# Kernel optimization log

Measured on AMD Instinct MI355X. Metric: run time of the kernel, lower is better.

Reference implementation:

```python
import jax, jax.numpy as jnp
import numpy as np

K, N = 4096, 4096
GROUP_SIZE = 64
N_GROUPS = N // GROUP_SIZE
B, S = 4, 2048
NBITS = 4


def setup_inputs() -> dict:
    key = jax.random.key(0)
    ks = jax.random.split(key, 7)
    x = jax.random.normal(ks[0], (B, S, N), dtype=jnp.float32)
    # per-group scales/zeros broadcast over the group_size axis
    scales = jax.random.uniform(ks[1], (K, N_GROUPS, 1), dtype=jnp.float32, minval=0.001, maxval=0.05)
    zeros = jax.random.uniform(ks[2], (K, N_GROUPS, 1), dtype=jnp.float32, minval=0.0, maxval=2.0 ** NBITS - 1)
    mu1 = jax.random.uniform(ks[3], (N,), dtype=jnp.float32, minval=0.5, maxval=1.5)
    mu2 = jax.random.uniform(ks[4], (K,), dtype=jnp.float32, minval=0.5, maxval=1.5)
    bias = jax.random.normal(ks[5], (K,), dtype=jnp.float32)
    W_q = jax.random.randint(ks[6], (K, N), 0, 2 ** NBITS, dtype=jnp.int32)
    return {"x": x, "scales": scales, "zeros": zeros, "mu1": mu1, "mu2": mu2, "bias": bias, "W_q": W_q}


def reference(x, scales, zeros, mu1, mu2, bias, W_q):
    # dequantize: per-group (Q - zero) * scale, then Sinkhorn rescale mu2 (rows) * mu1 (cols)
    k, n = W_q.shape
    n_groups = scales.shape[1]
    Qg = W_q.astype(jnp.float32).reshape(k, n_groups, -1)  # [K, G, gs]
    W_deq = ((Qg - zeros) * scales).reshape(k, n) * mu2[:, None] * mu1[None, :]
    W_deq = W_deq.astype(x.dtype)
    # nn.functional.linear: x @ W^T + b
    return jnp.einsum('bsn,kn->bsk', x, W_deq) + bias
```

## Files before the change

### kernel.cpp

```cpp
#include <hip/hip_runtime.h>
#include <hip/hip_bf16.h>
#include <stdint.h>
#include <type_traits>

typedef unsigned short u16;
typedef __bf16 bf16x8 __attribute__((ext_vector_type(8)));
typedef float f32x4 __attribute__((ext_vector_type(4)));

#define M_TOT 8192
#define N_TOT 4096
#define K_TOT 4096
#define BM 256
#define BN 256
#define BK 64
#define NT 64

#define HALF_EL 8192
#define B_OFF   16384
#define SLOT_EL 32768
#define SLOT_BYTES 65536

#define CVT_BLOCKS 16384
#define DEQ_BLOCKS 8192

template <int V> using ic = std::integral_constant<int, V>;
template <bool V> using bc = std::integral_constant<bool, V>;

__device__ __forceinline__ u16 f2bf(float f) {
    union { float f; uint32_t u; } v; v.f = f;
    uint32_t u = v.u;
    return (u16)((u + 0x7fffu + ((u >> 16) & 1u)) >> 16);
}

__global__ __launch_bounds__(256) void prep_kernel(const float* __restrict__ x,
                                                   u16* __restrict__ xb,
                                                   const int* __restrict__ wq,
                                                   const float* __restrict__ scales,
                                                   const float* __restrict__ zeros,
                                                   const float* __restrict__ mu1,
                                                   const float* __restrict__ mu2,
                                                   u16* __restrict__ wb) {
    const int b = blockIdx.x;
    if (b < CVT_BLOCKS) {
        const int i = b * 256 + threadIdx.x;
        const float4* p = (const float4*)x + (size_t)i * 2;
        float4 v0 = p[0], v1 = p[1];
        uint4 o;
        o.x = (uint32_t)f2bf(v0.x) | ((uint32_t)f2bf(v0.y) << 16);
        o.y = (uint32_t)f2bf(v0.z) | ((uint32_t)f2bf(v0.w) << 16);
        o.z = (uint32_t)f2bf(v1.x) | ((uint32_t)f2bf(v1.y) << 16);
        o.w = (uint32_t)f2bf(v1.z) | ((uint32_t)f2bf(v1.w) << 16);
        *((uint4*)(xb + (size_t)i * 8)) = o;
    } else {
        const int i = (b - CVT_BLOCKS) * 256 + threadIdx.x;
        const int k  = i >> 9;
        const int n0 = (i & 511) << 3;
        const int g  = n0 >> 6;
        const float z  = zeros[k * 64 + g];
        const float sm = scales[k * 64 + g] * mu2[k];
        const int4* qp = (const int4*)(wq + (size_t)k * N_TOT + n0);
        int4 q0 = qp[0], q1 = qp[1];
        const float4* mp = (const float4*)(mu1 + n0);
        float4 u0 = mp[0], u1 = mp[1];
        uint4 o;
        o.x = (uint32_t)f2bf(((float)q0.x - z) * sm * u0.x) |
              ((uint32_t)f2bf(((float)q0.y - z) * sm * u0.y) << 16);
        o.y = (uint32_t)f2bf(((float)q0.z - z) * sm * u0.z) |
              ((uint32_t)f2bf(((float)q0.w - z) * sm * u0.w) << 16);
        o.z = (uint32_t)f2bf(((float)q1.x - z) * sm * u1.x) |
              ((uint32_t)f2bf(((float)q1.y - z) * sm * u1.y) << 16);
        o.w = (uint32_t)f2bf(((float)q1.z - z) * sm * u1.z) |
              ((uint32_t)f2bf(((float)q1.w - z) * sm * u1.w) << 16);
        *((uint4*)(wb + (size_t)k * N_TOT + n0)) = o;
    }
}

__global__ __launch_bounds__(512, 2) void gemm_kernel(const u16* __restrict__ Xb,
                                                      const u16* __restrict__ Wb,
                                                      const float* __restrict__ bias,
                                                      float* __restrict__ out) {
    __shared__ __align__(16) u16 lds[2 * SLOT_EL];

    const int bid = blockIdx.x;
    const int cpx = gridDim.x >> 3;
    const int swz = (bid & 7) * cpx + (bid >> 3);
    const int bm = swz >> 4;
    const int bn = swz & 15;

    const int tid  = threadIdx.x;
    const int w    = tid >> 6;
    const int lane = tid & 63;
    const int wm = w >> 2, wn = w & 3;

    const int scol = (((lane & 7) ^ (lane >> 3)) << 3);
    const u16* aT = Xb + (size_t)(bm * BM + w * 16 + (lane >> 3)) * N_TOT + scol;
    const u16* bT = Wb + (size_t)(bn * BN + w * 16 + (lane >> 3)) * N_TOT + scol;

    u16* const sdA = &lds[w * 1024];
    u16* const sdB = &lds[B_OFF + w * 1024];

    auto gload = [](const u16* s, u16* d) {
        __builtin_amdgcn_global_load_lds(
            (const __attribute__((address_space(1))) uint32_t*)s,
            (__attribute__((address_space(3))) uint32_t*)d, 16, 0, 0);
    };
    auto stA = [&](auto SlC, auto Hc, auto Dc) {
        const u16* s = aT + (size_t)(Hc.value * 128) * N_TOT + Dc.value;
        u16* d = sdA + SlC.value * SLOT_EL + Hc.value * HALF_EL;
        gload(s, d); gload(s + (size_t)8 * N_TOT, d + 512);
    };
    auto stB = [&](auto SlC, auto Hc, auto Dc) {
        const u16* s = bT + (size_t)(Hc.value * 128) * N_TOT + Dc.value;
        u16* d = sdB + SlC.value * SLOT_EL + Hc.value * HALF_EL;
        gload(s, d); gload(s + (size_t)8 * N_TOT, d + 512);
    };

    const int cc0 = (((lane >> 4) << 3)) ^ ((lane & 7) << 3);
    const int rA  = ((wm << 4) + (lane & 15)) << 6;
    const int rB  = ((wn << 4) + (lane & 15)) << 6;
    int oAa = (rA + cc0) * 2;
    int oAb = (rA + (cc0 ^ 32)) * 2;
    int oBa = (B_OFF + rB + cc0) * 2;
    int oBb = (B_OFF + rB + (cc0 ^ 32)) * 2;
    const char* const ldsc = (const char*)lds;

    f32x4 acc[2][2][4][2] = {};
    bf16x8 afLo[4][2], afHi[4][2];
    bf16x8 bf0[2][2], bf1[2][2];

    auto rd_afLo_next = [&]() {
        const int xa = oAa ^ SLOT_BYTES, xb2 = oAb ^ SLOT_BYTES;
        #pragma unroll
        for (int j = 0; j < 4; ++j) {
            afLo[j][0] = *(const bf16x8*)(ldsc + xa + j * 4096);
            afLo[j][1] = *(const bf16x8*)(ldsc + xb2 + j * 4096);
        }
    };
    auto rd_bf0_next = [&]() {
        const int xa = oBa ^ SLOT_BYTES, xb2 = oBb ^ SLOT_BYTES;
        #pragma unroll
        for (int j2 = 0; j2 < 2; ++j2) {
            bf0[j2][0] = *(const bf16x8*)(ldsc + xa + j2 * 8192);
            bf0[j2][1] = *(const bf16x8*)(ldsc + xb2 + j2 * 8192);
        }
    };
    auto rd_afHi_cur = [&]() {
        #pragma unroll
        for (int j = 0; j < 4; ++j) {
            afHi[j][0] = *(const bf16x8*)(ldsc + oAa + 16384 + j * 4096);
            afHi[j][1] = *(const bf16x8*)(ldsc + oAb + 16384 + j * 4096);
        }
    };
    auto rd_bf1_cur = [&]() {
        #pragma unroll
        for (int j2 = 0; j2 < 2; ++j2) {
            bf1[j2][0] = *(const bf16x8*)(ldsc + oBa + 16384 + j2 * 8192);
            bf1[j2][1] = *(const bf16x8*)(ldsc + oBb + 16384 + j2 * 8192);
        }
    };

    #define MFMA_CLUSTER(A, B, MH, NH)                                          \
        __builtin_amdgcn_s_setprio(1);                                          \
        _Pragma("unroll")                                                       \
        for (int ks = 0; ks < 2; ++ks)                                          \
            _Pragma("unroll")                                                   \
            for (int j = 0; j < 4; ++j)                                         \
                _Pragma("unroll")                                               \
                for (int j2 = 0; j2 < 2; ++j2)                                  \
                    acc[MH][NH][j][j2] = __builtin_amdgcn_mfma_f32_16x16x32_bf16(\
                        A[j][ks], B[j2][ks], acc[MH][NH][j][j2], 0, 0, 0);      \
        __builtin_amdgcn_s_setprio(0);

    auto ktile = [&](auto SlC, auto St0, auto St2, auto RdN,
                     auto V1c, auto V3c, auto D0, auto D1) {
        constexpr int SL = SlC.value;
        rd_bf1_cur();
        if constexpr (St0.value) { stA(ic<SL ^ 1>{}, ic<1>{}, D0);
                                   stB(ic<SL ^ 1>{}, ic<1>{}, D0); }
        MFMA_CLUSTER(afLo, bf0, 0, 0)
        rd_afHi_cur();
        MFMA_CLUSTER(afLo, bf1, 0, 1)
        if constexpr (V1c.value == 4) asm volatile("s_waitcnt vmcnt(4)" ::: "memory");
        else if constexpr (V1c.value == 0) asm volatile("s_waitcnt vmcnt(0)" ::: "memory");
        __builtin_amdgcn_s_barrier();
        __builtin_amdgcn_sched_barrier(0);
        if constexpr (RdN.value) rd_afLo_next();
        if constexpr (St2.value) { stA(SlC, ic<0>{}, D1);
                                   stB(SlC, ic<0>{}, D1); }
        MFMA_CLUSTER(afHi, bf1, 1, 1)
        MFMA_CLUSTER(afHi, bf0, 1, 0)
        if constexpr (RdN.value) rd_bf0_next();
        if constexpr (V3c.value == 4) asm volatile("s_waitcnt vmcnt(4)" ::: "memory");
        else if constexpr (V3c.value == 0) asm volatile("s_waitcnt vmcnt(0)" ::: "memory");
        __builtin_amdgcn_s_barrier();
        __builtin_amdgcn_sched_barrier(0);
        oAa ^= SLOT_BYTES; oAb ^= SLOT_BYTES; oBa ^= SLOT_BYTES; oBb ^= SLOT_BYTES;
    };

    stA(ic<0>{}, ic<0>{}, ic<0>{});  stB(ic<0>{}, ic<0>{}, ic<0>{});
    stA(ic<0>{}, ic<1>{}, ic<0>{});  stB(ic<0>{}, ic<1>{}, ic<0>{});
    stA(ic<1>{}, ic<0>{}, ic<BK>{}); stB(ic<1>{}, ic<0>{}, ic<BK>{});
    asm volatile("s_waitcnt vmcnt(4)" ::: "memory");
    __builtin_amdgcn_s_barrier();
    __builtin_amdgcn_sched_barrier(0);
    {
        #pragma unroll
        for (int j = 0; j < 4; ++j) {
            afLo[j][0] = *(const bf16x8*)(ldsc + oAa + j * 4096);
            afLo[j][1] = *(const bf16x8*)(ldsc + oAb + j * 4096);
        }
        #pragma unroll
        for (int j2 = 0; j2 < 2; ++j2) {
            bf0[j2][0] = *(const bf16x8*)(ldsc + oBa + j2 * 8192);
            bf0[j2][1] = *(const bf16x8*)(ldsc + oBb + j2 * 8192);
        }
    }

    for (int it = 0; it < 31; ++it) {
        ktile(ic<0>{}, bc<true>{}, bc<true>{}, bc<true>{},
              ic<4>{}, ic<4>{}, ic<BK>{}, ic<2 * BK>{});
        ktile(ic<1>{}, bc<true>{}, bc<true>{}, bc<true>{},
              ic<4>{}, ic<4>{}, ic<2 * BK>{}, ic<3 * BK>{});
        aT += 2 * BK;
        bT += 2 * BK;
    }
    ktile(ic<0>{}, bc<true>{}, bc<false>{}, bc<true>{},
          ic<4>{}, ic<0>{}, ic<BK>{}, ic<0>{});
    ktile(ic<1>{}, bc<false>{}, bc<false>{}, bc<false>{},
          ic<-1>{}, ic<-1>{}, ic<0>{}, ic<0>{});

    #undef MFMA_CLUSTER

    #pragma unroll
    for (int mh_ = 0; mh_ < 2; ++mh_)
        #pragma unroll
        for (int j = 0; j < 4; ++j)
            #pragma unroll
            for (int rr = 0; rr < 4; ++rr) {
                const int row = bm * BM + mh_ * 128 + j * 32 + wm * 16 + ((lane >> 4) << 2) + rr;
                float* orow = out + (size_t)row * K_TOT;
                #pragma unroll
                for (int nh_ = 0; nh_ < 2; ++nh_)
                    #pragma unroll
                    for (int j2 = 0; j2 < 2; ++j2) {
                        const int col = bn * BN + nh_ * 128 + j2 * 64 + wn * 16 + (lane & 15);
                        orow[col] = acc[mh_][nh_][j][j2][rr] + bias[col];
                    }
            }
}

extern "C" void kernel_launch(void* const* d_in, const int* in_sizes, int n_in,
                              void* d_out, int out_size, void* d_ws, size_t ws_size,
                              hipStream_t stream) {
    const float* x      = (const float*)d_in[0];
    const float* scales = (const float*)d_in[1];
    const float* zeros  = (const float*)d_in[2];
    const float* mu1    = (const float*)d_in[3];
    const float* mu2    = (const float*)d_in[4];
    const float* bias   = (const float*)d_in[5];
    const int*   wq     = (const int*)d_in[6];
    float* out = (float*)d_out;

    u16* xb = (u16*)d_ws;
    u16* wb = (u16*)d_ws + (size_t)M_TOT * N_TOT;

    prep_kernel<<<CVT_BLOCKS + DEQ_BLOCKS, 256, 0, stream>>>(
        x, xb, wq, scales, zeros, mu1, mu2, wb);
    gemm_kernel<<<(M_TOT / BM) * (K_TOT / BN), 512, 0, stream>>>(xb, wb, bias, out);
}
```

Measured before the change: 264.9 us.

## Load weight operand directly from global into registers, stage only activations in LDS

The W tile is no longer staged through shared memory. Each wave now reads its B fragments straight from global memory into registers, one k-tile ahead, while only the X tile stays double-buffered in LDS. This halves LDS use and removes the B shared-memory writes, reads and the explicit vmcnt waits. In exchange, B loads are duplicated across waves that share columns, their latency is exposed to the compiler's own wait insertion, and the async A loads lose their explicit wait-count control.

```diff
diff --git a/kernel.cpp b/kernel.cpp
--- a/kernel.cpp
+++ b/kernel.cpp
@@ -16,9 +16,8 @@
 #define NT 64
 
 #define HALF_EL 8192
-#define B_OFF   16384
-#define SLOT_EL 32768
-#define SLOT_BYTES 65536
+#define ASLOT_EL 16384
+#define ASLOT_BYTES 32768
 
 #define CVT_BLOCKS 16384
 #define DEQ_BLOCKS 8192
@@ -79,7 +78,7 @@
                                                       const u16* __restrict__ Wb,
                                                       const float* __restrict__ bias,
                                                       float* __restrict__ out) {
-    __shared__ __align__(16) u16 lds[2 * SLOT_EL];
+    __shared__ __align__(16) u16 lds[2 * ASLOT_EL];
 
     const int bid = blockIdx.x;
     const int cpx = gridDim.x >> 3;
@@ -94,10 +93,8 @@
 
     const int scol = (((lane & 7) ^ (lane >> 3)) << 3);
     const u16* aT = Xb + (size_t)(bm * BM + w * 16 + (lane >> 3)) * N_TOT + scol;
-    const u16* bT = Wb + (size_t)(bn * BN + w * 16 + (lane >> 3)) * N_TOT + scol;
 
     u16* const sdA = &lds[w * 1024];
-    u16* const sdB = &lds[B_OFF + w * 1024];
 
     auto gload = [](const u16* s, u16* d) {
         __builtin_amdgcn_global_load_lds(
@@ -106,44 +103,34 @@
     };
     auto stA = [&](auto SlC, auto Hc, auto Dc) {
         const u16* s = aT + (size_t)(Hc.value * 128) * N_TOT + Dc.value;
-        u16* d = sdA + SlC.value * SLOT_EL + Hc.value * HALF_EL;
-        gload(s, d); gload(s + (size_t)8 * N_TOT, d + 512);
-    };
-    auto stB = [&](auto SlC, auto Hc, auto Dc) {
-        const u16* s = bT + (size_t)(Hc.value * 128) * N_TOT + Dc.value;
-        u16* d = sdB + SlC.value * SLOT_EL + Hc.value * HALF_EL;
+        u16* d = sdA + SlC.value * ASLOT_EL + Hc.value * HALF_EL;
         gload(s, d); gload(s + (size_t)8 * N_TOT, d + 512);
     };
 
     const int cc0 = (((lane >> 4) << 3)) ^ ((lane & 7) << 3);
     const int rA  = ((wm << 4) + (lane & 15)) << 6;
-    const int rB  = ((wn << 4) + (lane & 15)) << 6;
     int oAa = (rA + cc0) * 2;
     int oAb = (rA + (cc0 ^ 32)) * 2;
-    int oBa = (B_OFF + rB + cc0) * 2;
-    int oBb = (B_OFF + rB + (cc0 ^ 32)) * 2;
     const char* const ldsc = (const char*)lds;
+
+    const u16* pB00 = Wb + (size_t)(bn * BN + wn * 16 + (lane & 15)) * N_TOT
+                         + ((lane >> 4) << 3);
+    const u16* pB01 = pB00 + (size_t)64 * N_TOT;
+    const u16* pB10 = pB00 + (size_t)128 * N_TOT;
+    const u16* pB11 = pB00 + (size_t)192 * N_TOT;
 
     f32x4 acc[2][2][4][2] = {};
     bf16x8 afLo[4][2], afHi[4][2];
     bf16x8 bf0[2][2], bf1[2][2];
 
     auto rd_afLo_next = [&]() {
-        const int xa = oAa ^ SLOT_BYTES, xb2 = oAb ^ SLOT_BYTES;
+        const int xa = oAa ^ ASLOT_BYTES, xb2 = oAb ^ ASLOT_BYTES;
         #pragma unroll
         for (int j = 0; j < 4; ++j) {
             afLo[j][0] = *(const bf16x8*)(ldsc + xa + j * 4096);
             afLo[j][1] = *(const bf16x8*)(ldsc + xb2 + j * 4096);
         }
     };
-    auto rd_bf0_next = [&]() {
-        const int xa = oBa ^ SLOT_BYTES, xb2 = oBb ^ SLOT_BYTES;
-        #pragma unroll
-        for (int j2 = 0; j2 < 2; ++j2) {
-            bf0[j2][0] = *(const bf16x8*)(ldsc + xa + j2 * 8192);
-            bf0[j2][1] = *(const bf16x8*)(ldsc + xb2 + j2 * 8192);
-        }
-    };
     auto rd_afHi_cur = [&]() {
         #pragma unroll
         for (int j = 0; j < 4; ++j) {
@@ -151,11 +138,18 @@
             afHi[j][1] = *(const bf16x8*)(ldsc + oAb + 16384 + j * 4096);
         }
     };
-    auto rd_bf1_cur = [&]() {
-        #pragma unroll
-        for (int j2 = 0; j2 < 2; ++j2) {
-            bf1[j2][0] = *(const bf16x8*)(ldsc + oBa + 16384 + j2 * 8192);
-            bf1[j2][1] = *(const bf16x8*)(ldsc + oBb + 16384 + j2 * 8192);
+    auto rd_bf0_next = [&]() {
+        #pragma unroll
+        for (int ks = 0; ks < 2; ++ks) {
+            bf0[0][ks] = *(const bf16x8*)(pB00 + 64 + ks * 32);
+            bf0[1][ks] = *(const bf16x8*)(pB01 + 64 + ks * 32);
+        }
+    };
+    auto rd_bf1_next = [&]() {
+        #pragma unroll
+        for (int ks = 0; ks < 2; ++ks) {
+            bf1[0][ks] = *(const bf16x8*)(pB10 + 64 + ks * 32);
+            bf1[1][ks] = *(const bf16x8*)(pB11 + 64 + ks * 32);
         }
     };
 
@@ -171,36 +165,40 @@
                         A[j][ks], B[j2][ks], acc[MH][NH][j][j2], 0, 0, 0);      \
         __builtin_amdgcn_s_setprio(0);
 
-    auto ktile = [&](auto SlC, auto St0, auto St2, auto RdN,
-                     auto V1c, auto V3c, auto D0, auto D1) {
+    auto ktile = [&](auto SlC, auto St0, auto St2, auto RdN, auto D0, auto D1) {
         constexpr int SL = SlC.value;
-        rd_bf1_cur();
-        if constexpr (St0.value) { stA(ic<SL ^ 1>{}, ic<1>{}, D0);
-                                   stB(ic<SL ^ 1>{}, ic<1>{}, D0); }
+        if constexpr (St0.value) stA(ic<SL ^ 1>{}, ic<1>{}, D0);
         MFMA_CLUSTER(afLo, bf0, 0, 0)
         rd_afHi_cur();
         MFMA_CLUSTER(afLo, bf1, 0, 1)
-        if constexpr (V1c.value == 4) asm volatile("s_waitcnt vmcnt(4)" ::: "memory");
-        else if constexpr (V1c.value == 0) asm volatile("s_waitcnt vmcnt(0)" ::: "memory");
         __builtin_amdgcn_s_barrier();
         __builtin_amdgcn_sched_barrier(0);
         if constexpr (RdN.value) rd_afLo_next();
-        if constexpr (St2.value) { stA(SlC, ic<0>{}, D1);
-                                   stB(SlC, ic<0>{}, D1); }
-        MFMA_CLUSTER(afHi, bf1, 1, 1)
+        if constexpr (St2.value) stA(SlC, ic<0>{}, D1);
         MFMA_CLUSTER(afHi, bf0, 1, 0)
         if constexpr (RdN.value) rd_bf0_next();
-        if constexpr (V3c.value == 4) asm volatile("s_waitcnt vmcnt(4)" ::: "memory");
-        else if constexpr (V3c.value == 0) asm volatile("s_waitcnt vmcnt(0)" ::: "memory");
+        MFMA_CLUSTER(afHi, bf1, 1, 1)
+        if constexpr (RdN.value) rd_bf1_next();
         __builtin_amdgcn_s_barrier();
         __builtin_amdgcn_sched_barrier(0);
-        oAa ^= SLOT_BYTES; oAb ^= SLOT_BYTES; oBa ^= SLOT_BYTES; oBb ^= SLOT_BYTES;
-    };
-
-    stA(ic<0>{}, ic<0>{}, ic<0>{});  stB(ic<0>{}, ic<0>{}, ic<0>{});
-    stA(ic<0>{}, ic<1>{}, ic<0>{});  stB(ic<0>{}, ic<1>{}, ic<0>{});
-    stA(ic<1>{}, ic<0>{}, ic<BK>{}); stB(ic<1>{}, ic<0>{}, ic<BK>{});
-    asm volatile("s_waitcnt vmcnt(4)" ::: "memory");
+        oAa ^= ASLOT_BYTES; oAb ^= ASLOT_BYTES;
+        pB00 += 64; pB01 += 64; pB10 += 64; pB11 += 64;
+    };
+
+    stA(ic<0>{}, ic<0>{}, ic<0>{});
+    stA(ic<0>{}, ic<1>{}, ic<0>{});
+    stA(ic<1>{}, ic<0>{}, ic<BK>{});
+    #pragma unroll
+    for (int ks = 0; ks < 2; ++ks) {
+        bf0[0][ks] = *(const bf16x8*)(pB00 + ks * 32);
+        bf0[1][ks] = *(const bf16x8*)(pB01 + ks * 32);
+    }
+    #pragma unroll
+    for (int ks = 0; ks < 2; ++ks) {
+        bf1[0][ks] = *(const bf16x8*)(pB10 + ks * 32);
+        bf1[1][ks] = *(const bf16x8*)(pB11 + ks * 32);
+    }
+    asm volatile("s_waitcnt vmcnt(10)" ::: "memory");
     __builtin_amdgcn_s_barrier();
     __builtin_amdgcn_sched_barrier(0);
     {
@@ -209,25 +207,15 @@
             afLo[j][0] = *(const bf16x8*)(ldsc + oAa + j * 4096);
             afLo[j][1] = *(const bf16x8*)(ldsc + oAb + j * 4096);
         }
-        #pragma unroll
-        for (int j2 = 0; j2 < 2; ++j2) {
-            bf0[j2][0] = *(const bf16x8*)(ldsc + oBa + j2 * 8192);
-            bf0[j2][1] = *(const bf16x8*)(ldsc + oBb + j2 * 8192);
-        }
     }
 
     for (int it = 0; it < 31; ++it) {
-        ktile(ic<0>{}, bc<true>{}, bc<true>{}, bc<true>{},
-              ic<4>{}, ic<4>{}, ic<BK>{}, ic<2 * BK>{});
-        ktile(ic<1>{}, bc<true>{}, bc<true>{}, bc<true>{},
-              ic<4>{}, ic<4>{}, ic<2 * BK>{}, ic<3 * BK>{});
+        ktile(ic<0>{}, bc<true>{}, bc<true>{}, bc<true>{}, ic<BK>{},     ic<2 * BK>{});
+        ktile(ic<1>{}, bc<true>{}, bc<true>{}, bc<true>{}, ic<2 * BK>{}, ic<3 * BK>{});
         aT += 2 * BK;
-        bT += 2 * BK;
-    }
-    ktile(ic<0>{}, bc<true>{}, bc<false>{}, bc<true>{},
-          ic<4>{}, ic<0>{}, ic<BK>{}, ic<0>{});
-    ktile(ic<1>{}, bc<false>{}, bc<false>{}, bc<false>{},
-          ic<-1>{}, ic<-1>{}, ic<0>{}, ic<0>{});
+    }
+    ktile(ic<0>{}, bc<true>{}, bc<false>{}, bc<true>{}, ic<BK>{}, ic<0>{});
+    ktile(ic<1>{}, bc<false>{}, bc<false>{}, bc<false>{}, ic<0>{}, ic<0>{});
 
     #undef MFMA_CLUSTER
 
```

New measurement: 428.2 us. 61.7% more time.
